# Optimization experiments

Hardware: AMD Instinct MI355X
Metric: run time of the kernel (lower is better)

## Reference

```python
import jax, jax.numpy as jnp
import numpy as np

D_MODEL = 512

def setup_inputs() -> dict:
    key = jax.random.key(0)
    k1, k2, k3, k4, k5 = jax.random.split(key, 5)
    x = jax.random.normal(k1, (8, D_MODEL, 2048), dtype=jnp.float32)
    s = 1.0 / np.sqrt(D_MODEL)
    W_qkv = jax.random.uniform(k2, (D_MODEL, 3 * D_MODEL), dtype=jnp.float32, minval=-s, maxval=s)
    b_qkv = jax.random.uniform(k3, (3 * D_MODEL,), dtype=jnp.float32, minval=-s, maxval=s)
    W_proj = jax.random.uniform(k4, (D_MODEL, D_MODEL), dtype=jnp.float32, minval=-s, maxval=s)
    b_proj = jax.random.uniform(k5, (D_MODEL,), dtype=jnp.float32, minval=-s, maxval=s)
    return {"x": x, "W_qkv": W_qkv, "b_qkv": b_qkv, "W_proj": W_proj, "b_proj": b_proj}

def reference(x, W_qkv, b_qkv, W_proj, b_proj):
    # x: [B, L, N] with L == d_model; attend across the N variable axis
    xt = jnp.swapaxes(x, 1, 2)                      # [B, N, L]
    L = xt.shape[-1]
    qkv = xt @ W_qkv + b_qkv                        # [B, N, 3L]
    q, k, v = jnp.split(qkv, 3, axis=-1)            # each [B, N, L]
    attn = jnp.einsum('bnd,bmd->bnm', q, k) / jnp.sqrt(jnp.float32(L))
    attn = jax.nn.softmax(attn, axis=-1)            # [B, N, N]
    out = jnp.einsum('bnm,bmd->bnd', attn, v)       # [B, N, L]
    out = out @ W_proj + b_proj                     # [B, N, L]
    return jnp.swapaxes(out, 1, 2)                  # [B, L, N]
```

## Files before the change

### kernel.cpp

```cpp
#include <hip/hip_runtime.h>

#define NVAR 2048
#define DM   512
#define J3   1536

typedef _Float16 f16;
typedef _Float16 f16x8 __attribute__((ext_vector_type(8)));
typedef _Float16 f16x4 __attribute__((ext_vector_type(4)));
typedef float    f32x4 __attribute__((ext_vector_type(4)));

__global__ __launch_bounds__(256)
void k_tr(const float* __restrict__ src, f16* __restrict__ dst,
          int R, int C, long bsSrc, long bsDst) {
    __shared__ float t[64][65];
    const float* s = src + (size_t)blockIdx.z * bsSrc;
    f16* d = dst + (size_t)blockIdx.z * bsDst;
    const int c0 = blockIdx.x * 64, r0 = blockIdx.y * 64;
    const int tx = threadIdx.x & 63, w = threadIdx.x >> 6;
#pragma unroll
    for (int i = 0; i < 16; ++i) {
        int r = w * 16 + i;
        t[r][tx] = s[(size_t)(r0 + r) * C + c0 + tx];
    }
    __syncthreads();
#pragma unroll
    for (int i = 0; i < 16; ++i) {
        int c = w * 16 + i;
        d[(size_t)(c0 + c) * R + r0 + tx] = (f16)t[tx][c];
    }
}

template<int MODE>
__global__ __launch_bounds__(256)
void gemm_f16(const f16* __restrict__ A, const f16* __restrict__ B,
              long bsA, long bsB, int lda, int ldb, int K, int nbx,
              const float* __restrict__ bias, float scale,
              f16* __restrict__ o0, f16* __restrict__ o1, f16* __restrict__ o2,
              float* __restrict__ of) {
    __shared__ f16 sA[128 * 64];
    __shared__ f16 sB[128 * 64];
    const int tid  = threadIdx.x;
    const int lane = tid & 63;
    const int w    = __builtin_amdgcn_readfirstlane(tid >> 6);
    const int wm   = (w >> 1) * 64;
    const int wn   = (w & 1) * 64;
    const int z    = blockIdx.x;
    const int bid  = blockIdx.y;
    const int bxA  = bid % nbx;
    const int bxB  = bid / nbx;

    const f16* Ab = A + (size_t)z * bsA + (size_t)bxA * 128 * lda;
    const f16* Bb = B + (size_t)z * bsB + (size_t)bxB * 128 * ldb;

    int srcA[4], srcB[4];
#pragma unroll
    for (int i = 0; i < 4; ++i) {
        int slot = i * 256 + tid;
        int row  = slot >> 3;
        int s    = (slot & 7) ^ (row & 7);
        srcA[i] = row * lda + s * 8;
        srcB[i] = row * ldb + s * 8;
    }

    f32x4 acc[4][4] = {};
    float rs[4] = {};

    for (int k0 = 0; k0 < K; k0 += 64) {
        __syncthreads();
#pragma unroll
        for (int i = 0; i < 4; ++i) {
            __builtin_amdgcn_global_load_lds(
                (const __attribute__((address_space(1))) void*)(Ab + srcA[i] + k0),
                (__attribute__((address_space(3))) void*)(sA + i * 2048 + w * 512),
                16, 0, 0);
            __builtin_amdgcn_global_load_lds(
                (const __attribute__((address_space(1))) void*)(Bb + srcB[i] + k0),
                (__attribute__((address_space(3))) void*)(sB + i * 2048 + w * 512),
                16, 0, 0);
        }
        __syncthreads();
#pragma unroll
        for (int kh = 0; kh < 2; ++kh) {
            f16x8 av[4], bv[4];
#pragma unroll
            for (int mi = 0; mi < 4; ++mi) {
                int r = wm + mi * 16 + (lane & 15);
                int s = (kh * 4 + (lane >> 4)) ^ (r & 7);
                av[mi] = *(const f16x8*)(sA + r * 64 + s * 8);
            }
#pragma unroll
            for (int nj = 0; nj < 4; ++nj) {
                int r = wn + nj * 16 + (lane & 15);
                int s = (kh * 4 + (lane >> 4)) ^ (r & 7);
                bv[nj] = *(const f16x8*)(sB + r * 64 + s * 8);
            }
            if constexpr (MODE == 2) {
#pragma unroll
                for (int nj = 0; nj < 4; ++nj)
#pragma unroll
                    for (int e = 0; e < 8; ++e)
                        rs[nj] += (float)bv[nj][e];
            }
#pragma unroll
            for (int mi = 0; mi < 4; ++mi)
#pragma unroll
                for (int nj = 0; nj < 4; ++nj)
                    acc[mi][nj] = __builtin_amdgcn_mfma_f32_16x16x32_f16(
                        av[mi], bv[nj], acc[mi][nj], 0, 0, 0);
        }
    }

    const int rb0 = bxA * 128 + wm + (lane >> 4) * 4;
    const int cb0 = bxB * 128 + wn + (lane & 15);

    if (MODE == 0) {
        const int seg = (bxA * 128) >> 9;
#pragma unroll
        for (int mi = 0; mi < 4; ++mi) {
            const int j = rb0 + mi * 16;
            const f32x4 b4 = *(const f32x4*)(bias + j);
#pragma unroll
            for (int nj = 0; nj < 4; ++nj) {
                const int n = cb0 + nj * 16;
                if (seg == 2) {
#pragma unroll
                    for (int r = 0; r < 4; ++r)
                        o2[((size_t)z * DM + (j - 1024 + r)) * NVAR + n] =
                            (f16)(acc[mi][nj][r] + b4[r]);
                } else {
                    f16* dst = seg ? o1 : o0;
                    const int jj = seg ? j - 512 : j;
                    f16x4 vv;
#pragma unroll
                    for (int r = 0; r < 4; ++r) vv[r] = (f16)(acc[mi][nj][r] + b4[r]);
                    *(f16x4*)(dst + ((size_t)z * NVAR + n) * DM + jj) = vv;
                }
            }
        }
    } else if (MODE == 1) {
#pragma unroll
        for (int mi = 0; mi < 4; ++mi)
#pragma unroll
            for (int nj = 0; nj < 4; ++nj) {
                f16x4 vv;
#pragma unroll
                for (int r = 0; r < 4; ++r)
                    vv[r] = (f16)__expf(acc[mi][nj][r] * scale);
                *(f16x4*)(o0 + ((size_t)z * NVAR + cb0 + nj * 16) * NVAR
                               + rb0 + mi * 16) = vv;
            }
    } else if (MODE == 2) {
#pragma unroll
        for (int nj = 0; nj < 4; ++nj) {
            rs[nj] += __shfl_xor(rs[nj], 16);
            rs[nj] += __shfl_xor(rs[nj], 32);
            rs[nj] = 1.0f / rs[nj];
        }
#pragma unroll
        for (int mi = 0; mi < 4; ++mi)
#pragma unroll
            for (int nj = 0; nj < 4; ++nj) {
                f16x4 vv;
#pragma unroll
                for (int r = 0; r < 4; ++r)
                    vv[r] = (f16)(acc[mi][nj][r] * rs[nj]);
                *(f16x4*)(o0 + ((size_t)z * NVAR + cb0 + nj * 16) * DM
                               + rb0 + mi * 16) = vv;
            }
    } else {
#pragma unroll
        for (int mi = 0; mi < 4; ++mi)
#pragma unroll
            for (int nj = 0; nj < 4; ++nj) {
                const int l = cb0 + nj * 16;
                const float bb = bias[l];
                f32x4 vv;
#pragma unroll
                for (int r = 0; r < 4; ++r) vv[r] = acc[mi][nj][r] + bb;
                *(f32x4*)(of + ((size_t)z * DM + l) * NVAR + rb0 + mi * 16) = vv;
            }
    }
}

extern "C" void kernel_launch(void* const* d_in, const int* in_sizes, int n_in,
                              void* d_out, int out_size, void* d_ws, size_t ws_size,
                              hipStream_t stream) {
    const float* x     = (const float*)d_in[0];
    const float* Wqkv  = (const float*)d_in[1];
    const float* bqkv  = (const float*)d_in[2];
    const float* Wproj = (const float*)d_in[3];
    const float* bproj = (const float*)d_in[4];
    float* out = (float*)d_out;

    const size_t PB = (size_t)NVAR * DM;
    f16* xT  = (f16*)d_ws;
    f16* q   = xT + 8 * PB;
    f16* kk  = q  + 8 * PB;
    f16* vT  = kk + 8 * PB;
    f16* S   = vT + 8 * PB;
    f16* O   = S  + (size_t)8 * NVAR * NVAR;
    f16* WqT = O  + 8 * PB;
    f16* WpT = WqT + (size_t)J3 * DM;

    k_tr<<<dim3(NVAR / 64, DM / 64, 8), 256, 0, stream>>>(
        x, xT, DM, NVAR, (long)DM * NVAR, (long)NVAR * DM);
    k_tr<<<dim3(J3 / 64, DM / 64, 1), 256, 0, stream>>>(Wqkv, WqT, DM, J3, 0, 0);
    k_tr<<<dim3(DM / 64, DM / 64, 1), 256, 0, stream>>>(Wproj, WpT, DM, DM, 0, 0);

    gemm_f16<0><<<dim3(8, 12 * 16), 256, 0, stream>>>(
        WqT, xT, 0, (long)NVAR * DM, DM, DM, DM, 12,
        bqkv, 1.f, q, kk, vT, nullptr);

    gemm_f16<1><<<dim3(8, 16 * 16), 256, 0, stream>>>(
        kk, q, (long)NVAR * DM, (long)NVAR * DM, DM, DM, DM, 16,
        nullptr, 0.044194173824159216f, S, nullptr, nullptr, nullptr);

    gemm_f16<2><<<dim3(8, 4 * 16), 256, 0, stream>>>(
        vT, S, (long)DM * NVAR, (long)NVAR * NVAR, NVAR, NVAR, NVAR, 4,
        nullptr, 1.f, O, nullptr, nullptr, nullptr);

    gemm_f16<3><<<dim3(8, 16 * 4), 256, 0, stream>>>(
        O, WpT, (long)NVAR * DM, 0, DM, DM, DM, 16,
        bproj, 1.f, nullptr, nullptr, nullptr, out);
}
```

Before: 185.4 us.

## Double-buffer LDS tiles in the f16 GEMM to overlap loads with MFMA

Splits the shared-memory A/B tiles into two buffers. The next K tile is issued with global_load_lds while MFMAs run on the current tile, so each step now needs one vmcnt wait and one barrier instead of two syncthreads around the load. Wave priority is raised during the MFMA section. The cost is that LDS per block doubles to 64KB, which may lower the number of blocks resident per CU.

```diff
diff --git a/kernel.cpp b/kernel.cpp
--- a/kernel.cpp
+++ b/kernel.cpp
@@ -8,6 +8,11 @@
 typedef _Float16 f16x8 __attribute__((ext_vector_type(8)));
 typedef _Float16 f16x4 __attribute__((ext_vector_type(4)));
 typedef float    f32x4 __attribute__((ext_vector_type(4)));
+
+#define SBAR() do { asm volatile("s_barrier" ::: "memory"); \
+                    __builtin_amdgcn_sched_barrier(0); } while(0)
+#define WAITVM0() do { asm volatile("s_waitcnt vmcnt(0)" ::: "memory"); \
+                       __builtin_amdgcn_sched_barrier(0); } while(0)
 
 __global__ __launch_bounds__(256)
 void k_tr(const float* __restrict__ src, f16* __restrict__ dst,
@@ -37,8 +42,8 @@
               const float* __restrict__ bias, float scale,
               f16* __restrict__ o0, f16* __restrict__ o1, f16* __restrict__ o2,
               float* __restrict__ of) {
-    __shared__ f16 sA[128 * 64];
-    __shared__ f16 sB[128 * 64];
+    __shared__ f16 sA[2][128 * 64];
+    __shared__ f16 sB[2][128 * 64];
     const int tid  = threadIdx.x;
     const int lane = tid & 63;
     const int w    = __builtin_amdgcn_readfirstlane(tid >> 6);
@@ -62,23 +67,38 @@
         srcB[i] = row * ldb + s * 8;
     }
 
+    auto STAGE = [&](int kt) {
+        f16* dA = sA[kt & 1];
+        f16* dB = sB[kt & 1];
+        const int k0 = kt * 64;
+#pragma unroll
+        for (int i = 0; i < 4; ++i)
+            __builtin_amdgcn_global_load_lds(
+                (const __attribute__((address_space(1))) void*)(Ab + srcA[i] + k0),
+                (__attribute__((address_space(3))) void*)(dA + i * 2048 + w * 512),
+                16, 0, 0);
+#pragma unroll
+        for (int i = 0; i < 4; ++i)
+            __builtin_amdgcn_global_load_lds(
+                (const __attribute__((address_space(1))) void*)(Bb + srcB[i] + k0),
+                (__attribute__((address_space(3))) void*)(sB[kt & 1] + i * 2048 + w * 512),
+                16, 0, 0);
+        (void)dB;
+    };
+
     f32x4 acc[4][4] = {};
     float rs[4] = {};
-
-    for (int k0 = 0; k0 < K; k0 += 64) {
-        __syncthreads();
-#pragma unroll
-        for (int i = 0; i < 4; ++i) {
-            __builtin_amdgcn_global_load_lds(
-                (const __attribute__((address_space(1))) void*)(Ab + srcA[i] + k0),
-                (__attribute__((address_space(3))) void*)(sA + i * 2048 + w * 512),
-                16, 0, 0);
-            __builtin_amdgcn_global_load_lds(
-                (const __attribute__((address_space(1))) void*)(Bb + srcB[i] + k0),
-                (__attribute__((address_space(3))) void*)(sB + i * 2048 + w * 512),
-                16, 0, 0);
-        }
-        __syncthreads();
+    const int NT = K >> 6;
+
+    STAGE(0);
+    WAITVM0();
+    SBAR();
+
+    for (int t = 0; t < NT; ++t) {
+        const f16* pA = sA[t & 1];
+        const f16* pB = sB[t & 1];
+        if (t + 1 < NT) STAGE(t + 1);
+        __builtin_amdgcn_s_setprio(1);
 #pragma unroll
         for (int kh = 0; kh < 2; ++kh) {
             f16x8 av[4], bv[4];
@@ -86,13 +106,13 @@
             for (int mi = 0; mi < 4; ++mi) {
                 int r = wm + mi * 16 + (lane & 15);
                 int s = (kh * 4 + (lane >> 4)) ^ (r & 7);
-                av[mi] = *(const f16x8*)(sA + r * 64 + s * 8);
+                av[mi] = *(const f16x8*)(pA + r * 64 + s * 8);
             }
 #pragma unroll
             for (int nj = 0; nj < 4; ++nj) {
                 int r = wn + nj * 16 + (lane & 15);
                 int s = (kh * 4 + (lane >> 4)) ^ (r & 7);
-                bv[nj] = *(const f16x8*)(sB + r * 64 + s * 8);
+                bv[nj] = *(const f16x8*)(pB + r * 64 + s * 8);
             }
             if constexpr (MODE == 2) {
 #pragma unroll
@@ -107,6 +127,11 @@
                 for (int nj = 0; nj < 4; ++nj)
                     acc[mi][nj] = __builtin_amdgcn_mfma_f32_16x16x32_f16(
                         av[mi], bv[nj], acc[mi][nj], 0, 0, 0);
+        }
+        __builtin_amdgcn_s_setprio(0);
+        if (t + 1 < NT) {
+            WAITVM0();
+            SBAR();
         }
     }
 
```

Result: slower. 192.5 us (+3.8%).

## Replace GEMM with 8-wave double-buffered pipelined kernel and larger tiles

Applied to the files above, without the earlier changes.

Replaces the single-buffered 128x128 GEMM with an 8-wave, 512-thread template that double-buffers LDS and stages A/B in half-tiles. Explicit vmcnt waits and barriers let global-to-LDS loads for later k-tiles overlap MFMA work on the current tile. Tiles grow to 128x256 or 256x256 per block, and MFMA sections raise wave priority. This targets load latency exposed by the two syncthreads per k-step and improves operand reuse. In exchange it uses more LDS and registers, and its hand-counted wait logic is fragile.

```diff
diff --git a/kernel.cpp b/kernel.cpp
--- a/kernel.cpp
+++ b/kernel.cpp
@@ -8,6 +8,36 @@
 typedef _Float16 f16x8 __attribute__((ext_vector_type(8)));
 typedef _Float16 f16x4 __attribute__((ext_vector_type(4)));
 typedef float    f32x4 __attribute__((ext_vector_type(4)));
+
+#define SBAR() do { asm volatile("s_barrier" ::: "memory"); \
+                    __builtin_amdgcn_sched_barrier(0); } while(0)
+#define LGKM0() do { asm volatile("s_waitcnt lgkmcnt(0)" ::: "memory"); \
+                     __builtin_amdgcn_sched_barrier(0); } while(0)
+#define GLOAD(gp, lp) __builtin_amdgcn_global_load_lds( \
+    (const __attribute__((address_space(1))) void*)(gp), \
+    (__attribute__((address_space(3))) void*)(lp), 16, 0, 0)
+
+__device__ __forceinline__ void waitvm_n(int n) {
+    switch (n) {
+    case 0:  asm volatile("s_waitcnt vmcnt(0)"  ::: "memory"); break;
+    case 1:  asm volatile("s_waitcnt vmcnt(1)"  ::: "memory"); break;
+    case 2:  asm volatile("s_waitcnt vmcnt(2)"  ::: "memory"); break;
+    case 3:  asm volatile("s_waitcnt vmcnt(3)"  ::: "memory"); break;
+    case 4:  asm volatile("s_waitcnt vmcnt(4)"  ::: "memory"); break;
+    case 5:  asm volatile("s_waitcnt vmcnt(5)"  ::: "memory"); break;
+    case 6:  asm volatile("s_waitcnt vmcnt(6)"  ::: "memory"); break;
+    case 7:  asm volatile("s_waitcnt vmcnt(7)"  ::: "memory"); break;
+    case 8:  asm volatile("s_waitcnt vmcnt(8)"  ::: "memory"); break;
+    case 9:  asm volatile("s_waitcnt vmcnt(9)"  ::: "memory"); break;
+    case 10: asm volatile("s_waitcnt vmcnt(10)" ::: "memory"); break;
+    case 11: asm volatile("s_waitcnt vmcnt(11)" ::: "memory"); break;
+    case 12: asm volatile("s_waitcnt vmcnt(12)" ::: "memory"); break;
+    case 13: asm volatile("s_waitcnt vmcnt(13)" ::: "memory"); break;
+    case 14: asm volatile("s_waitcnt vmcnt(14)" ::: "memory"); break;
+    default: break;
+    }
+    __builtin_amdgcn_sched_barrier(0);
+}
 
 __global__ __launch_bounds__(256)
 void k_tr(const float* __restrict__ src, f16* __restrict__ dst,
@@ -30,97 +60,171 @@
     }
 }
 
-template<int MODE>
-__global__ __launch_bounds__(256)
-void gemm_f16(const f16* __restrict__ A, const f16* __restrict__ B,
-              long bsA, long bsB, int lda, int ldb, int K, int nbx,
-              const float* __restrict__ bias, float scale,
-              f16* __restrict__ o0, f16* __restrict__ o1, f16* __restrict__ o2,
-              float* __restrict__ of) {
-    __shared__ f16 sA[128 * 64];
-    __shared__ f16 sB[128 * 64];
+template<int BM, int BN, int WGM, int MODE>
+__global__ __launch_bounds__(512, 2)
+void gemm8(const f16* __restrict__ A, const f16* __restrict__ B,
+           long bsA, long bsB, int lda, int ldb, int K, int nbx,
+           const float* __restrict__ bias, float scale,
+           f16* __restrict__ o0, f16* __restrict__ o1, f16* __restrict__ o2,
+           float* __restrict__ of) {
+    constexpr int WGN = 8 / WGM;
+    constexpr int WTM = BM / WGM, WTN = BN / WGN;
+    constexpr int MI = WTM / 16, NJ = WTN / 16, MIH = MI / 2, NJH = NJ / 2;
+    constexpr int LA = BM / 128, LB = BN / 128;
+    constexpr int HA = BM / 2, HB = BN / 2;
+
+    __shared__ f16 sA[2 * BM * 64];
+    __shared__ f16 sB[2 * BN * 64];
+
     const int tid  = threadIdx.x;
     const int lane = tid & 63;
     const int w    = __builtin_amdgcn_readfirstlane(tid >> 6);
-    const int wm   = (w >> 1) * 64;
-    const int wn   = (w & 1) * 64;
+    const int wm   = (w / WGN) * WTM;
+    const int wn   = (w % WGN) * WTN;
     const int z    = blockIdx.x;
     const int bid  = blockIdx.y;
     const int bxA  = bid % nbx;
     const int bxB  = bid / nbx;
 
-    const f16* Ab = A + (size_t)z * bsA + (size_t)bxA * 128 * lda;
-    const f16* Bb = B + (size_t)z * bsB + (size_t)bxB * 128 * ldb;
-
-    int srcA[4], srcB[4];
-#pragma unroll
-    for (int i = 0; i < 4; ++i) {
-        int slot = i * 256 + tid;
-        int row  = slot >> 3;
-        int s    = (slot & 7) ^ (row & 7);
-        srcA[i] = row * lda + s * 8;
-        srcB[i] = row * ldb + s * 8;
-    }
-
-    f32x4 acc[4][4] = {};
-    float rs[4] = {};
-
-    for (int k0 = 0; k0 < K; k0 += 64) {
-        __syncthreads();
-#pragma unroll
-        for (int i = 0; i < 4; ++i) {
-            __builtin_amdgcn_global_load_lds(
-                (const __attribute__((address_space(1))) void*)(Ab + srcA[i] + k0),
-                (__attribute__((address_space(3))) void*)(sA + i * 2048 + w * 512),
-                16, 0, 0);
-            __builtin_amdgcn_global_load_lds(
-                (const __attribute__((address_space(1))) void*)(Bb + srcB[i] + k0),
-                (__attribute__((address_space(3))) void*)(sB + i * 2048 + w * 512),
-                16, 0, 0);
-        }
-        __syncthreads();
-#pragma unroll
-        for (int kh = 0; kh < 2; ++kh) {
-            f16x8 av[4], bv[4];
-#pragma unroll
-            for (int mi = 0; mi < 4; ++mi) {
-                int r = wm + mi * 16 + (lane & 15);
-                int s = (kh * 4 + (lane >> 4)) ^ (r & 7);
-                av[mi] = *(const f16x8*)(sA + r * 64 + s * 8);
-            }
-#pragma unroll
-            for (int nj = 0; nj < 4; ++nj) {
-                int r = wn + nj * 16 + (lane & 15);
-                int s = (kh * 4 + (lane >> 4)) ^ (r & 7);
-                bv[nj] = *(const f16x8*)(sB + r * 64 + s * 8);
-            }
-            if constexpr (MODE == 2) {
-#pragma unroll
-                for (int nj = 0; nj < 4; ++nj)
+    const f16* Ab = A + (size_t)z * bsA + (size_t)bxA * BM * lda;
+    const f16* Bb = B + (size_t)z * bsB + (size_t)bxB * BN * ldb;
+
+    auto STG_A = [&](int kt, int h, int p) {
+        f16* d = sA + p * (BM * 64) + h * (HA * 64);
+        const int k0 = kt * 64;
+#pragma unroll
+        for (int i = 0; i < LA; ++i) {
+            int slot = i * 512 + tid;
+            int r = h * HA + (slot >> 3);
+            int s = (slot & 7) ^ (r & 7);
+            GLOAD(Ab + (size_t)r * lda + s * 8 + k0, d + slot * 8);
+        }
+    };
+    auto STG_B = [&](int kt, int h, int p) {
+        f16* d = sB + p * (BN * 64) + h * (HB * 64);
+        const int k0 = kt * 64;
+#pragma unroll
+        for (int i = 0; i < LB; ++i) {
+            int slot = i * 512 + tid;
+            int r = h * HB + (slot >> 3);
+            int s = (slot & 7) ^ (r & 7);
+            GLOAD(Bb + (size_t)r * ldb + s * 8 + k0, d + slot * 8);
+        }
+    };
+
+    int koff[2];
+#pragma unroll
+    for (int ks = 0; ks < 2; ++ks)
+        koff[ks] = ((ks * 4 + (lane >> 4)) ^ (lane & 7)) * 8;
+    const int rowA = (wm + (lane & 15)) * 64;
+    const int rowB = (wn + (lane & 15)) * 64;
+
+    f16x8 av[MI][2], bv[NJ][2];
+    f32x4 acc[MI][NJ] = {};
+    float rs[NJ] = {};
+
+    auto LD_AV = [&](const f16* p, int mi0) {
+#pragma unroll
+        for (int mi = 0; mi < MIH; ++mi)
+#pragma unroll
+            for (int ks = 0; ks < 2; ++ks)
+                av[mi0 + mi][ks] = *(const f16x8*)(p + rowA + (mi0 + mi) * 1024 + koff[ks]);
+    };
+    auto LD_BV = [&](const f16* p, int nj0) {
+#pragma unroll
+        for (int nj = 0; nj < NJH; ++nj)
+#pragma unroll
+            for (int ks = 0; ks < 2; ++ks)
+                bv[nj0 + nj][ks] = *(const f16x8*)(p + rowB + (nj0 + nj) * 1024 + koff[ks]);
+    };
+    auto SUMB = [&](int nj0) {
+        if constexpr (MODE == 2) {
+#pragma unroll
+            for (int nj = 0; nj < NJH; ++nj)
+#pragma unroll
+                for (int ks = 0; ks < 2; ++ks)
 #pragma unroll
                     for (int e = 0; e < 8; ++e)
-                        rs[nj] += (float)bv[nj][e];
-            }
-#pragma unroll
-            for (int mi = 0; mi < 4; ++mi)
-#pragma unroll
-                for (int nj = 0; nj < 4; ++nj)
-                    acc[mi][nj] = __builtin_amdgcn_mfma_f32_16x16x32_f16(
-                        av[mi], bv[nj], acc[mi][nj], 0, 0, 0);
-        }
-    }
-
-    const int rb0 = bxA * 128 + wm + (lane >> 4) * 4;
-    const int cb0 = bxB * 128 + wn + (lane & 15);
+                        rs[nj0 + nj] += (float)bv[nj0 + nj][ks][e];
+        }
+    };
+    auto MM = [&](int mi0, int nj0) {
+        __builtin_amdgcn_s_setprio(1);
+#pragma unroll
+        for (int mi = 0; mi < MIH; ++mi)
+#pragma unroll
+            for (int nj = 0; nj < NJH; ++nj)
+#pragma unroll
+                for (int ks = 0; ks < 2; ++ks)
+                    acc[mi0 + mi][nj0 + nj] = __builtin_amdgcn_mfma_f32_16x16x32_f16(
+                        av[mi0 + mi][ks], bv[nj0 + nj][ks], acc[mi0 + mi][nj0 + nj], 0, 0, 0);
+        __builtin_amdgcn_s_setprio(0);
+    };
+
+    const int NT = K >> 6;
+    int issued = 0, stampAhi[2], stampBhi[2];
+
+    STG_A(0, 0, 0); issued += LA;
+    STG_A(0, 1, 0); issued += LA; stampAhi[0] = issued;
+    STG_B(0, 0, 0); issued += LB;
+    STG_B(0, 1, 0); issued += LB; stampBhi[0] = issued;
+    STG_A(1, 0, 1); issued += LA;
+    STG_A(1, 1, 1); issued += LA; stampAhi[1] = issued;
+    STG_B(1, 0, 1); issued += LB;
+    stampBhi[1] = 0;
+    waitvm_n(issued - stampBhi[0]);
+    SBAR();
+    LD_AV(sA, 0);
+    LD_BV(sB, NJH);
+    LGKM0();
+    SUMB(NJH);
+
+#define TILE_BODY(t, P) { \
+    const f16* pA  = sA + (P) * (BM * 64); \
+    const f16* pB  = sB + (P) * (BN * 64); \
+    const f16* pA2 = sA + (1 - (P)) * (BM * 64); \
+    const f16* pB2 = sB + (1 - (P)) * (BN * 64); \
+     \
+    waitvm_n(issued - stampBhi[P]); SBAR(); \
+    if ((t) + 1 < NT) { STG_B((t) + 1, 1, 1 - (P)); issued += LB; stampBhi[1 - (P)] = issued; } \
+    LD_BV(pB, 0); LGKM0(); SUMB(0); MM(0, 0); \
+     \
+    waitvm_n(issued - stampAhi[P]); SBAR(); \
+    if ((t) + 2 < NT) { STG_B((t) + 2, 0, (P)); issued += LB; } \
+    LD_AV(pA, MIH); LGKM0(); MM(0, NJH); \
+     \
+    if ((t) + 1 < NT) { \
+        waitvm_n(issued - stampAhi[1 - (P)]); SBAR(); \
+        if ((t) + 2 < NT) { STG_A((t) + 2, 0, (P)); issued += LA; } \
+        LD_AV(pA2, 0); LGKM0(); \
+    } \
+    MM(MIH, NJH); \
+     \
+    if ((t) + 1 < NT) { \
+        waitvm_n(issued - stampBhi[1 - (P)]); SBAR(); \
+        if ((t) + 2 < NT) { STG_A((t) + 2, 1, (P)); issued += LA; stampAhi[P] = issued; } \
+        LD_BV(pB2, NJH); LGKM0(); SUMB(NJH); \
+    } \
+    MM(MIH, 0); \
+}
+
+    for (int tt = 0; tt < NT; tt += 2) {
+        TILE_BODY(tt, 0);
+        TILE_BODY(tt + 1, 1);
+    }
+#undef TILE_BODY
+
+    const int rb0 = bxA * BM + wm + (lane >> 4) * 4;
+    const int cb0 = bxB * BN + wn + (lane & 15);
 
     if (MODE == 0) {
-        const int seg = (bxA * 128) >> 9;
-#pragma unroll
-        for (int mi = 0; mi < 4; ++mi) {
+        const int seg = (bxA * BM) >> 9;
+#pragma unroll
+        for (int mi = 0; mi < MI; ++mi) {
             const int j = rb0 + mi * 16;
             const f32x4 b4 = *(const f32x4*)(bias + j);
 #pragma unroll
-            for (int nj = 0; nj < 4; ++nj) {
+            for (int nj = 0; nj < NJ; ++nj) {
                 const int n = cb0 + nj * 16;
                 if (seg == 2) {
 #pragma unroll
@@ -139,9 +243,9 @@
         }
     } else if (MODE == 1) {
 #pragma unroll
-        for (int mi = 0; mi < 4; ++mi)
-#pragma unroll
-            for (int nj = 0; nj < 4; ++nj) {
+        for (int mi = 0; mi < MI; ++mi)
+#pragma unroll
+            for (int nj = 0; nj < NJ; ++nj) {
                 f16x4 vv;
 #pragma unroll
                 for (int r = 0; r < 4; ++r)
@@ -151,15 +255,15 @@
             }
     } else if (MODE == 2) {
 #pragma unroll
-        for (int nj = 0; nj < 4; ++nj) {
+        for (int nj = 0; nj < NJ; ++nj) {
             rs[nj] += __shfl_xor(rs[nj], 16);
             rs[nj] += __shfl_xor(rs[nj], 32);
             rs[nj] = 1.0f / rs[nj];
         }
 #pragma unroll
-        for (int mi = 0; mi < 4; ++mi)
-#pragma unroll
-            for (int nj = 0; nj < 4; ++nj) {
+        for (int mi = 0; mi < MI; ++mi)
+#pragma unroll
+            for (int nj = 0; nj < NJ; ++nj) {
                 f16x4 vv;
 #pragma unroll
                 for (int r = 0; r < 4; ++r)
@@ -169,9 +273,9 @@
             }
     } else {
 #pragma unroll
-        for (int mi = 0; mi < 4; ++mi)
-#pragma unroll
-            for (int nj = 0; nj < 4; ++nj) {
+        for (int mi = 0; mi < MI; ++mi)
+#pragma unroll
+            for (int nj = 0; nj < NJ; ++nj) {
                 const int l = cb0 + nj * 16;
                 const float bb = bias[l];
                 f32x4 vv;
@@ -207,19 +311,19 @@
     k_tr<<<dim3(J3 / 64, DM / 64, 1), 256, 0, stream>>>(Wqkv, WqT, DM, J3, 0, 0);
     k_tr<<<dim3(DM / 64, DM / 64, 1), 256, 0, stream>>>(Wproj, WpT, DM, DM, 0, 0);
 
-    gemm_f16<0><<<dim3(8, 12 * 16), 256, 0, stream>>>(
+    gemm8<128, 256, 2, 0><<<dim3(8, 12 * 8), 512, 0, stream>>>(
         WqT, xT, 0, (long)NVAR * DM, DM, DM, DM, 12,
         bqkv, 1.f, q, kk, vT, nullptr);
 
-    gemm_f16<1><<<dim3(8, 16 * 16), 256, 0, stream>>>(
-        kk, q, (long)NVAR * DM, (long)NVAR * DM, DM, DM, DM, 16,
+    gemm8<256, 256, 2, 1><<<dim3(8, 8 * 8), 512, 0, stream>>>(
+        kk, q, (long)NVAR * DM, (long)NVAR * DM, DM, DM, DM, 8,
         nullptr, 0.044194173824159216f, S, nullptr, nullptr, nullptr);
 
-    gemm_f16<2><<<dim3(8, 4 * 16), 256, 0, stream>>>(
+    gemm8<128, 256, 2, 2><<<dim3(8, 4 * 8), 512, 0, stream>>>(
         vT, S, (long)DM * NVAR, (long)NVAR * NVAR, NVAR, NVAR, NVAR, 4,
         nullptr, 1.f, O, nullptr, nullptr, nullptr);
 
-    gemm_f16<3><<<dim3(8, 16 * 4), 256, 0, stream>>>(
-        O, WpT, (long)NVAR * DM, 0, DM, DM, DM, 16,
+    gemm8<256, 128, 4, 3><<<dim3(8, 8 * 4), 512, 0, stream>>>(
+        O, WpT, (long)NVAR * DM, 0, DM, DM, DM, 8,
         bproj, 1.f, nullptr, nullptr, nullptr, out);
 }
```

New measurement: 219.7 us. +18.5%, slower.

## Use 256x256 tiles for QKV and score GEMMs and MFMA-based row sums

Applied to the files above, without the earlier changes.

Adds a 512-thread GEMM kernel that computes a 256x256 output tile per block, with B fragments held across two A half-passes, and uses it for the QKV projection and the QK^T score/exp stage. The larger tiles raise arithmetic intensity and cut repeated global loads, at the cost of more registers and LDS per block and fewer blocks (384 and 512) to fill the GPU. The PV stage now gets the softmax denominators from an extra MFMA against a vector of ones instead of scalar f16-to-f32 adds. This moves the row-sum work from VALU onto the matrix units.

```diff
diff --git a/kernel.cpp b/kernel.cpp
--- a/kernel.cpp
+++ b/kernel.cpp
@@ -8,6 +8,10 @@
 typedef _Float16 f16x8 __attribute__((ext_vector_type(8)));
 typedef _Float16 f16x4 __attribute__((ext_vector_type(4)));
 typedef float    f32x4 __attribute__((ext_vector_type(4)));
+
+#define GLOAD(gp, lp) __builtin_amdgcn_global_load_lds( \
+    (const __attribute__((address_space(1))) void*)(gp), \
+    (__attribute__((address_space(3))) void*)(lp), 16, 0, 0)
 
 __global__ __launch_bounds__(256)
 void k_tr(const float* __restrict__ src, f16* __restrict__ dst,
@@ -31,12 +35,128 @@
 }
 
 template<int MODE>
+__global__ __launch_bounds__(512, 2)
+void gemm_big(const f16* __restrict__ A, const f16* __restrict__ B,
+              long bsA, long bsB, int lda, int ldb, int K, int nbx,
+              const float* __restrict__ bias, float scale,
+              f16* __restrict__ o0, f16* __restrict__ o1, f16* __restrict__ o2) {
+    __shared__ f16 sA[256 * 64];
+    __shared__ f16 sB[256 * 64];
+    const int tid  = threadIdx.x;
+    const int lane = tid & 63;
+    const int w    = __builtin_amdgcn_readfirstlane(tid >> 6);
+    const int wm   = (w >> 2) * 128;
+    const int wn   = (w & 3) * 64;
+    const int z    = blockIdx.x;
+    const int bid  = blockIdx.y;
+    const int bxA  = bid % nbx;
+    const int bxB  = bid / nbx;
+
+    const f16* Ab = A + (size_t)z * bsA + (size_t)bxA * 256 * lda;
+    const f16* Bb = B + (size_t)z * bsB + (size_t)bxB * 256 * ldb;
+
+    int srcA[4], srcB[4];
+#pragma unroll
+    for (int i = 0; i < 4; ++i) {
+        int slot = i * 512 + tid;
+        int row  = slot >> 3;
+        int s    = (slot & 7) ^ (row & 7);
+        srcA[i] = row * lda + s * 8;
+        srcB[i] = row * ldb + s * 8;
+    }
+
+    int koff[2];
+#pragma unroll
+    for (int ks = 0; ks < 2; ++ks)
+        koff[ks] = ((ks * 4 + (lane >> 4)) ^ (lane & 7)) * 8;
+    const int rowA = (wm + (lane & 15)) * 64;
+    const int rowB = (wn + (lane & 15)) * 64;
+
+    f32x4 acc[8][4] = {};
+
+    for (int k0 = 0; k0 < K; k0 += 64) {
+        __syncthreads();
+#pragma unroll
+        for (int i = 0; i < 4; ++i)
+            GLOAD(Ab + srcA[i] + k0, sA + i * 4096 + w * 512);
+#pragma unroll
+        for (int i = 0; i < 4; ++i)
+            GLOAD(Bb + srcB[i] + k0, sB + i * 4096 + w * 512);
+        __syncthreads();
+
+        f16x8 bv[4][2];
+#pragma unroll
+        for (int nj = 0; nj < 4; ++nj)
+#pragma unroll
+            for (int ks = 0; ks < 2; ++ks)
+                bv[nj][ks] = *(const f16x8*)(sB + rowB + nj * 1024 + koff[ks]);
+#pragma unroll
+        for (int h = 0; h < 2; ++h) {
+            f16x8 av[4][2];
+#pragma unroll
+            for (int mi = 0; mi < 4; ++mi)
+#pragma unroll
+                for (int ks = 0; ks < 2; ++ks)
+                    av[mi][ks] = *(const f16x8*)(sA + rowA + (h * 4 + mi) * 1024 + koff[ks]);
+#pragma unroll
+            for (int mi = 0; mi < 4; ++mi)
+#pragma unroll
+                for (int nj = 0; nj < 4; ++nj)
+#pragma unroll
+                    for (int ks = 0; ks < 2; ++ks)
+                        acc[h * 4 + mi][nj] = __builtin_amdgcn_mfma_f32_16x16x32_f16(
+                            av[mi][ks], bv[nj][ks], acc[h * 4 + mi][nj], 0, 0, 0);
+        }
+    }
+
+    const int rb0 = bxA * 256 + wm + (lane >> 4) * 4;
+    const int cb0 = bxB * 256 + wn + (lane & 15);
+
+    if (MODE == 0) {
+        const int seg = (bxA * 256) >> 9;
+#pragma unroll
+        for (int mi = 0; mi < 8; ++mi) {
+            const int j = rb0 + mi * 16;
+            const f32x4 b4 = *(const f32x4*)(bias + j);
+#pragma unroll
+            for (int nj = 0; nj < 4; ++nj) {
+                const int n = cb0 + nj * 16;
+                if (seg == 2) {
+#pragma unroll
+                    for (int r = 0; r < 4; ++r)
+                        o2[((size_t)z * DM + (j - 1024 + r)) * NVAR + n] =
+                            (f16)(acc[mi][nj][r] + b4[r]);
+                } else {
+                    f16* dst = seg ? o1 : o0;
+                    const int jj = seg ? j - 512 : j;
+                    f16x4 vv;
+#pragma unroll
+                    for (int r = 0; r < 4; ++r) vv[r] = (f16)(acc[mi][nj][r] + b4[r]);
+                    *(f16x4*)(dst + ((size_t)z * NVAR + n) * DM + jj) = vv;
+                }
+            }
+        }
+    } else {
+#pragma unroll
+        for (int mi = 0; mi < 8; ++mi)
+#pragma unroll
+            for (int nj = 0; nj < 4; ++nj) {
+                f16x4 vv;
+#pragma unroll
+                for (int r = 0; r < 4; ++r)
+                    vv[r] = (f16)__expf(acc[mi][nj][r] * scale);
+                *(f16x4*)(o0 + ((size_t)z * NVAR + cb0 + nj * 16) * NVAR
+                               + rb0 + mi * 16) = vv;
+            }
+    }
+}
+
+template<int MODE>
 __global__ __launch_bounds__(256)
 void gemm_f16(const f16* __restrict__ A, const f16* __restrict__ B,
               long bsA, long bsB, int lda, int ldb, int K, int nbx,
               const float* __restrict__ bias, float scale,
-              f16* __restrict__ o0, f16* __restrict__ o1, f16* __restrict__ o2,
-              float* __restrict__ of) {
+              f16* __restrict__ o0, float* __restrict__ of) {
     __shared__ f16 sA[128 * 64];
     __shared__ f16 sB[128 * 64];
     const int tid  = threadIdx.x;
@@ -62,21 +182,19 @@
         srcB[i] = row * ldb + s * 8;
     }
 
+    f16x8 ones;
+#pragma unroll
+    for (int e = 0; e < 8; ++e) ones[e] = (f16)1.0f;
+
     f32x4 acc[4][4] = {};
-    float rs[4] = {};
+    f32x4 accrs[4] = {};
 
     for (int k0 = 0; k0 < K; k0 += 64) {
         __syncthreads();
 #pragma unroll
         for (int i = 0; i < 4; ++i) {
-            __builtin_amdgcn_global_load_lds(
-                (const __attribute__((address_space(1))) void*)(Ab + srcA[i] + k0),
-                (__attribute__((address_space(3))) void*)(sA + i * 2048 + w * 512),
-                16, 0, 0);
-            __builtin_amdgcn_global_load_lds(
-                (const __attribute__((address_space(1))) void*)(Bb + srcB[i] + k0),
-                (__attribute__((address_space(3))) void*)(sB + i * 2048 + w * 512),
-                16, 0, 0);
+            GLOAD(Ab + srcA[i] + k0, sA + i * 2048 + w * 512);
+            GLOAD(Bb + srcB[i] + k0, sB + i * 2048 + w * 512);
         }
         __syncthreads();
 #pragma unroll
@@ -97,9 +215,8 @@
             if constexpr (MODE == 2) {
 #pragma unroll
                 for (int nj = 0; nj < 4; ++nj)
-#pragma unroll
-                    for (int e = 0; e < 8; ++e)
-                        rs[nj] += (float)bv[nj][e];
+                    accrs[nj] = __builtin_amdgcn_mfma_f32_16x16x32_f16(
+                        ones, bv[nj], accrs[nj], 0, 0, 0);
             }
 #pragma unroll
             for (int mi = 0; mi < 4; ++mi)
@@ -113,31 +230,10 @@
     const int rb0 = bxA * 128 + wm + (lane >> 4) * 4;
     const int cb0 = bxB * 128 + wn + (lane & 15);
 
-    if (MODE == 0) {
-        const int seg = (bxA * 128) >> 9;
-#pragma unroll
-        for (int mi = 0; mi < 4; ++mi) {
-            const int j = rb0 + mi * 16;
-            const f32x4 b4 = *(const f32x4*)(bias + j);
-#pragma unroll
-            for (int nj = 0; nj < 4; ++nj) {
-                const int n = cb0 + nj * 16;
-                if (seg == 2) {
-#pragma unroll
-                    for (int r = 0; r < 4; ++r)
-                        o2[((size_t)z * DM + (j - 1024 + r)) * NVAR + n] =
-                            (f16)(acc[mi][nj][r] + b4[r]);
-                } else {
-                    f16* dst = seg ? o1 : o0;
-                    const int jj = seg ? j - 512 : j;
-                    f16x4 vv;
-#pragma unroll
-                    for (int r = 0; r < 4; ++r) vv[r] = (f16)(acc[mi][nj][r] + b4[r]);
-                    *(f16x4*)(dst + ((size_t)z * NVAR + n) * DM + jj) = vv;
-                }
-            }
-        }
-    } else if (MODE == 1) {
+    if (MODE == 2) {
+        float inv[4];
+#pragma unroll
+        for (int nj = 0; nj < 4; ++nj) inv[nj] = 1.0f / accrs[nj][0];
 #pragma unroll
         for (int mi = 0; mi < 4; ++mi)
 #pragma unroll
@@ -145,25 +241,7 @@
                 f16x4 vv;
 #pragma unroll
                 for (int r = 0; r < 4; ++r)
-                    vv[r] = (f16)__expf(acc[mi][nj][r] * scale);
-                *(f16x4*)(o0 + ((size_t)z * NVAR + cb0 + nj * 16) * NVAR
-                               + rb0 + mi * 16) = vv;
-            }
-    } else if (MODE == 2) {
-#pragma unroll
-        for (int nj = 0; nj < 4; ++nj) {
-            rs[nj] += __shfl_xor(rs[nj], 16);
-            rs[nj] += __shfl_xor(rs[nj], 32);
-            rs[nj] = 1.0f / rs[nj];
-        }
-#pragma unroll
-        for (int mi = 0; mi < 4; ++mi)
-#pragma unroll
-            for (int nj = 0; nj < 4; ++nj) {
-                f16x4 vv;
-#pragma unroll
-                for (int r = 0; r < 4; ++r)
-                    vv[r] = (f16)(acc[mi][nj][r] * rs[nj]);
+                    vv[r] = (f16)(acc[mi][nj][r] * inv[nj]);
                 *(f16x4*)(o0 + ((size_t)z * NVAR + cb0 + nj * 16) * DM
                                + rb0 + mi * 16) = vv;
             }
@@ -207,19 +285,19 @@
     k_tr<<<dim3(J3 / 64, DM / 64, 1), 256, 0, stream>>>(Wqkv, WqT, DM, J3, 0, 0);
     k_tr<<<dim3(DM / 64, DM / 64, 1), 256, 0, stream>>>(Wproj, WpT, DM, DM, 0, 0);
 
-    gemm_f16<0><<<dim3(8, 12 * 16), 256, 0, stream>>>(
-        WqT, xT, 0, (long)NVAR * DM, DM, DM, DM, 12,
-        bqkv, 1.f, q, kk, vT, nullptr);
-
-    gemm_f16<1><<<dim3(8, 16 * 16), 256, 0, stream>>>(
-        kk, q, (long)NVAR * DM, (long)NVAR * DM, DM, DM, DM, 16,
-        nullptr, 0.044194173824159216f, S, nullptr, nullptr, nullptr);
+    gemm_big<0><<<dim3(8, 6 * 8), 512, 0, stream>>>(
+        WqT, xT, 0, (long)NVAR * DM, DM, DM, DM, 6,
+        bqkv, 1.f, q, kk, vT);
+
+    gemm_big<1><<<dim3(8, 8 * 8), 512, 0, stream>>>(
+        kk, q, (long)NVAR * DM, (long)NVAR * DM, DM, DM, DM, 8,
+        nullptr, 0.044194173824159216f, S, nullptr, nullptr);
 
     gemm_f16<2><<<dim3(8, 4 * 16), 256, 0, stream>>>(
         vT, S, (long)DM * NVAR, (long)NVAR * NVAR, NVAR, NVAR, NVAR, 4,
-        nullptr, 1.f, O, nullptr, nullptr, nullptr);
+        nullptr, 1.f, O, nullptr);
 
     gemm_f16<3><<<dim3(8, 16 * 4), 256, 0, stream>>>(
         O, WpT, (long)NVAR * DM, 0, DM, DM, DM, 16,
-        bproj, 1.f, nullptr, nullptr, nullptr, out);
+        bproj, 1.f, nullptr, out);
 }
```

New measurement: 185.5 us. Within noise of the previous version (+0.0%).
